# Kernel tuning notes

Hardware: AMD Instinct MI355X
Metric: run time of the kernel (lower is better)

Reference implementation:

```python
import jax, jax.numpy as jnp
import numpy as np


def _rank_transform_ascending(flat):
    # torch: _, idx = sort(flat, descending=False); flat[idx] = linspace(0,1,n)+1/n
    n = flat.shape[0]
    order = jnp.argsort(flat)  # ascending
    prob = jnp.linspace(0.0, 1.0, n, dtype=flat.dtype) + jnp.asarray(1.0 / n, flat.dtype)
    return jnp.zeros_like(flat).at[order].set(prob)


def corr_attention(query, key, value):
    # score[b,h,i,j] = cosine-like similarity q_i . k_j / (|q_i| |k_j|)
    score = jnp.einsum('bhid,bhjd->bhij', query, key)
    q_len = jnp.sqrt(jnp.sum(query * query, axis=-1, keepdims=True)) + 1e-5  # [b,h,s,1]
    k_len = jnp.sqrt(jnp.sum(key * key, axis=-1, keepdims=True)) + 1e-5      # [b,h,s,1]
    score = score / (q_len * jnp.swapaxes(k_len, -1, -2))
    signal = jnp.sign(score)
    size = score.shape
    flat = jnp.abs(score).reshape(-1)
    ranked = _rank_transform_ascending(flat)
    score = -jnp.log(ranked).reshape(size) * signal
    score = score / jnp.sum(jnp.abs(score), axis=-1, keepdims=True)
    return jnp.einsum('bhij,bhjd->bhid', score, value)


def setup_inputs() -> dict:
    key0 = jax.random.key(0)
    kq, kk, kv = jax.random.split(key0, 3)
    B, H, S, D = 4, 8, 1024, 64
    query = jax.random.normal(kq, (B, H, S, D), dtype=jnp.float32)
    key = jax.random.normal(kk, (B, H, S, D), dtype=jnp.float32)
    value = jax.random.normal(kv, (B, H, S, D), dtype=jnp.float32)
    return {"query": query, "key": key, "value": value}


def reference(query, key, value):
    # Attention.forward with mode='season'
    return corr_attention(query, key, value)
```

## Files before the change

kernel.cpp:

```cpp
#include <hip/hip_runtime.h>
#include <math.h>
#include <stdint.h>

#define S_LEN 1024
#define D_DIM 64
#define BH    32
#define KSHIFT 13
#define NBINS 130048u
#define HOT_LO 115712u
#define NHOT   14336u
#define HIST_LO 117760u
#define NHOT_H  12288u
#define NCHUNK 254
#define HBLK   256
#define INV_NM1 (1.0f/33554431.0f)
#define INV_N   (2.9802322387695312e-08f)
#define FIX_TH  1e-4f

typedef _Float16 half8 __attribute__((ext_vector_type(8)));
typedef short    short8 __attribute__((ext_vector_type(8)));
typedef float    floatx4 __attribute__((ext_vector_type(4)));

__global__ __launch_bounds__(256) void norms_kernel(
    const float* __restrict__ Q, const float* __restrict__ K,
    double* __restrict__ qinvD, double* __restrict__ kinvD,
    float* __restrict__ qinvF, float* __restrict__ kinvF) {
  int row  = blockIdx.x * 4 + (threadIdx.x >> 6);
  int lane = threadIdx.x & 63;
  const float* src; double* dstD; float* dstF; int r = row;
  if (row < BH * S_LEN) { src = Q; dstD = qinvD; dstF = qinvF; }
  else                  { src = K; dstD = kinvD; dstF = kinvF; r = row - BH * S_LEN; }
  double v = (double)src[(size_t)r * D_DIM + lane];
  double s = v * v;
  #pragma unroll
  for (int off = 32; off; off >>= 1) s += __shfl_down(s, off);
  if (lane == 0) {
    double inv = 1.0 / (sqrt(s) + 1e-5);
    dstD[r] = inv;
    dstF[r] = (float)inv;
  }
}

__device__ __forceinline__ void bf16_split(float x, short& hi, short& lo) {
  unsigned u = __float_as_uint(x);
  unsigned h = (u + 0x7FFFu + ((u >> 16) & 1u)) >> 16;
  float hf = __uint_as_float(h << 16);
  float lf = x - hf;
  hi = (short)h;
  lo = (short)(__float_as_uint(lf) >> 16);
}

__global__ __launch_bounds__(256) void qk_mfma_kernel(
    const float* __restrict__ Q, const float* __restrict__ K,
    const float* __restrict__ qinvF, const float* __restrict__ kinvF,
    float* __restrict__ score) {
  __shared__ short Qhi[64][72], Qlo[64][72];
  __shared__ short Khi[64][72], Klo[64][72];
  int bh = blockIdx.z;
  int i0 = blockIdx.y * 64;
  int j0 = blockIdx.x * 64;
  int tid = threadIdx.x;
  const float* Qb = Q + ((size_t)bh * S_LEN + i0) * D_DIM;
  const float* Kb = K + ((size_t)bh * S_LEN + j0) * D_DIM;
  #pragma unroll
  for (int l = 0; l < 4; ++l) {
    int idx4 = l * 256 + tid;
    int row  = idx4 >> 4;
    int c4   = idx4 & 15;
    float qi = qinvF[(size_t)bh * S_LEN + i0 + row];
    float4 v = ((const float4*)Qb)[idx4];
    float qv[4] = {v.x * qi, v.y * qi, v.z * qi, v.w * qi};
    short qh[4], ql[4];
    #pragma unroll
    for (int c = 0; c < 4; ++c) bf16_split(qv[c], qh[c], ql[c]);
    *(short4*)&Qhi[row][c4 * 4] = make_short4(qh[0], qh[1], qh[2], qh[3]);
    *(short4*)&Qlo[row][c4 * 4] = make_short4(ql[0], ql[1], ql[2], ql[3]);
    float kj = kinvF[(size_t)bh * S_LEN + j0 + row];
    float4 w = ((const float4*)Kb)[idx4];
    float kv[4] = {w.x * kj, w.y * kj, w.z * kj, w.w * kj};
    short kh[4], kl[4];
    #pragma unroll
    for (int c = 0; c < 4; ++c) bf16_split(kv[c], kh[c], kl[c]);
    *(short4*)&Khi[row][c4 * 4] = make_short4(kh[0], kh[1], kh[2], kh[3]);
    *(short4*)&Klo[row][c4 * 4] = make_short4(kl[0], kl[1], kl[2], kl[3]);
  }
  __syncthreads();
  int wave = tid >> 6;
  int lane = tid & 63;
  int m    = lane & 15;
  int quad = lane >> 4;
  floatx4 acc[4];
  #pragma unroll
  for (int n = 0; n < 4; ++n) acc[n] = (floatx4){0.f, 0.f, 0.f, 0.f};
  #pragma unroll
  for (int ks = 0; ks < 2; ++ks) {
    int kb = ks * 32 + quad * 8;
    short8 a_hi = *(const short8*)&Qhi[wave * 16 + m][kb];
    short8 a_lo = *(const short8*)&Qlo[wave * 16 + m][kb];
    #pragma unroll
    for (int nt = 0; nt < 4; ++nt) {
      short8 b_hi = *(const short8*)&Khi[nt * 16 + m][kb];
      short8 b_lo = *(const short8*)&Klo[nt * 16 + m][kb];
      acc[nt] = __builtin_amdgcn_mfma_f32_16x16x32_bf16(a_hi, b_hi, acc[nt], 0, 0, 0);
      acc[nt] = __builtin_amdgcn_mfma_f32_16x16x32_bf16(a_hi, b_lo, acc[nt], 0, 0, 0);
      acc[nt] = __builtin_amdgcn_mfma_f32_16x16x32_bf16(a_lo, b_hi, acc[nt], 0, 0, 0);
    }
  }
  #pragma unroll
  for (int r = 0; r < 4; ++r) {
    float* op = score + ((size_t)bh * S_LEN + i0 + wave * 16 + quad * 4 + r) * S_LEN + j0 + m;
    #pragma unroll
    for (int nt = 0; nt < 4; ++nt)
      op[nt * 16] = acc[nt][r];
  }
}

__global__ __launch_bounds__(1024) void hist_kernel(
    float* __restrict__ score, const float* __restrict__ Q, const float* __restrict__ K,
    const double* __restrict__ qinvD, const double* __restrict__ kinvD,
    unsigned* __restrict__ hist, unsigned char* __restrict__ partial) {
  __shared__ unsigned lh[NHOT_H];
  int tid = threadIdx.x;
  int lane = tid & 63;
  for (unsigned i = tid; i < NHOT_H; i += 1024) lh[i] = 0u;
  __syncthreads();
  const float4* p = (const float4*)score + (size_t)blockIdx.x * 32768;
  #pragma unroll 2
  for (int it = 0; it < 32; ++it) {
    float4 v = p[it * 1024 + tid];
    float vv[4] = {v.x, v.y, v.z, v.w};
    bool anyf = (fabsf(vv[0]) < FIX_TH) | (fabsf(vv[1]) < FIX_TH) |
                (fabsf(vv[2]) < FIX_TH) | (fabsf(vv[3]) < FIX_TH);
    unsigned long long am = __ballot(anyf);
    while (am) {
      int src = (int)(__ffsll((long long)am) - 1);
      am &= am - 1;
      unsigned base4 = (unsigned)(blockIdx.x * 32768u + (unsigned)(it * 1024 + tid));
      unsigned b4 = __shfl(base4, src);
      #pragma unroll
      for (int c = 0; c < 4; ++c) {
        float sc = __shfl(vv[c], src);
        if (fabsf(sc) < FIX_TH) {
          unsigned flat = b4 * 4u + (unsigned)c;
          unsigned bh = flat >> 20, i = (flat >> 10) & 1023u, j = flat & 1023u;
          double qd = (double)Q[((size_t)bh * S_LEN + i) * D_DIM + lane];
          double kd = (double)K[((size_t)bh * S_LEN + j) * D_DIM + lane];
          double pd = qd * kd;
          #pragma unroll
          for (int off = 32; off; off >>= 1) pd += __shfl_down(pd, off);
          float corr = 0.f;
          if (lane == 0)
            corr = (float)(pd * qinvD[(size_t)bh * S_LEN + i] * kinvD[(size_t)bh * S_LEN + j]);
          corr = __shfl(corr, 0);
          if (lane == src) {
            vv[c] = corr;
            score[(size_t)flat] = corr;
          }
        }
      }
    }
    #pragma unroll
    for (int c = 0; c < 4; ++c) {
      unsigned b = __float_as_uint(fabsf(vv[c])) >> KSHIFT;
      if (b >= NBINS) b = NBINS - 1u;
      if (b >= HIST_LO) atomicAdd(&lh[b - HIST_LO], 1u);
      else              atomicAdd(&hist[b], 1u);
    }
  }
  __syncthreads();
  unsigned char* dst = partial + (size_t)blockIdx.x * NHOT_H;
  for (unsigned i = tid; i < NHOT_H; i += 1024) dst[i] = (unsigned char)lh[i];
}

__global__ __launch_bounds__(256) void hreduce_kernel(
    const unsigned char* __restrict__ partial, unsigned* __restrict__ hist) {
  unsigned bin = blockIdx.x * 256 + threadIdx.x;
  unsigned s = 0;
  #pragma unroll 8
  for (int b = 0; b < HBLK; ++b) s += (unsigned)partial[(size_t)b * NHOT_H + bin];
  hist[HIST_LO + bin] = s;
}

__global__ __launch_bounds__(256) void vt_kernel(
    const float* __restrict__ V, _Float16* __restrict__ Vt) {
  __shared__ _Float16 T[64][72];
  int bh = blockIdx.y, j0 = blockIdx.x * 64, tid = threadIdx.x;
  const float* Vb = V + ((size_t)bh * S_LEN + j0) * D_DIM;
  #pragma unroll
  for (int l = 0; l < 4; ++l) {
    int idx = l * 256 + tid;
    int jr = idx >> 4, d4 = idx & 15;
    float4 v = ((const float4*)Vb)[idx];
    T[d4*4+0][jr] = (_Float16)v.x;
    T[d4*4+1][jr] = (_Float16)v.y;
    T[d4*4+2][jr] = (_Float16)v.z;
    T[d4*4+3][jr] = (_Float16)v.w;
  }
  __syncthreads();
  _Float16* Ob = Vt + (size_t)bh * D_DIM * S_LEN + j0;
  #pragma unroll
  for (int l = 0; l < 2; ++l) {
    int idx = l * 256 + tid;
    int d = idx >> 3, jc = idx & 7;
    uint4 val = *(const uint4*)&T[d][jc*8];
    *(uint4*)(Ob + (size_t)d * S_LEN + jc*8) = val;
  }
}

__global__ __launch_bounds__(256) void scan1_kernel(const unsigned* __restrict__ hist,
                                                    unsigned* __restrict__ csum) {
  __shared__ unsigned sd[256];
  int c = blockIdx.x, t = threadIdx.x;
  const unsigned* p = hist + (size_t)c * 512;
  sd[t] = p[t] + p[t + 256];
  __syncthreads();
  for (int off = 128; off; off >>= 1) {
    if (t < off) sd[t] += sd[t + off];
    __syncthreads();
  }
  if (t == 0) csum[c] = sd[0];
}

__global__ __launch_bounds__(256) void scan2_kernel(unsigned* __restrict__ csum) {
  __shared__ unsigned d[256];
  int t = threadIdx.x;
  unsigned v = (t < NCHUNK) ? csum[t] : 0u;
  d[t] = v; __syncthreads();
  for (int off = 1; off < 256; off <<= 1) {
    unsigned x = (t >= off) ? d[t - off] : 0u;
    __syncthreads();
    d[t] += x;
    __syncthreads();
  }
  if (t < NCHUNK) csum[t] = d[t] - v;
}

__global__ __launch_bounds__(256) void scan3_kernel(const unsigned* __restrict__ hist,
                                                    const unsigned* __restrict__ csum,
                                                    _Float16* __restrict__ tTab16) {
  __shared__ unsigned ts[256];
  int c = blockIdx.x, t = threadIdx.x;
  const unsigned* p = hist + (size_t)c * 512 + t * 2;
  unsigned l0 = p[0], l1 = p[1];
  unsigned s = l0 + l1;
  ts[t] = s; __syncthreads();
  for (int off = 1; off < 256; off <<= 1) {
    unsigned x = (t >= off) ? ts[t - off] : 0u;
    __syncthreads();
    ts[t] += x;
    __syncthreads();
  }
  unsigned base = csum[c] + ts[t] - s;
  int idx = c * 512 + t * 2;
  float r0 = (float)base + 0.5f * ((float)l0 - 1.0f);
  tTab16[idx]     = (_Float16)(-__logf(fmaf(r0, INV_NM1, INV_N)));
  float r1 = (float)(base + l0) + 0.5f * ((float)l1 - 1.0f);
  tTab16[idx + 1] = (_Float16)(-__logf(fmaf(r1, INV_NM1, INV_N)));
}

__global__ __launch_bounds__(256, 2) void pv_mfma_kernel(
    const float* __restrict__ score, const _Float16* __restrict__ Vt,
    const unsigned short* __restrict__ tTab16, float* __restrict__ out) {
  __shared__ unsigned short ldsT[NHOT];
  int tid = threadIdx.x;
  {
    const unsigned* gsrc = (const unsigned*)(tTab16 + HOT_LO);
    unsigned* ldst = (unsigned*)ldsT;
    #pragma unroll
    for (int i = 0; i < 28; ++i)
      ldst[i * 256 + tid] = gsrc[i * 256 + tid];
  }
  __syncthreads();

  int bh   = blockIdx.y;
  int wave = tid >> 6;
  int lane = tid & 63;
  int m    = lane & 15;
  int quad = lane >> 4;
  int i0   = blockIdx.x * 64 + wave * 16;
  const float*    Sb = score + ((size_t)bh * S_LEN + i0 + m) * S_LEN;
  const _Float16* Vb = Vt + (size_t)bh * D_DIM * S_LEN;
  floatx4 acc[4];
  #pragma unroll
  for (int n = 0; n < 4; ++n) acc[n] = (floatx4){0.f, 0.f, 0.f, 0.f};
  float rsum = 0.f;

  auto gather8 = [&](const float4& a, const float4& b, unsigned short* t8) {
    float sv[8] = {a.x, a.y, a.z, a.w, b.x, b.y, b.z, b.w};
    #pragma unroll
    for (int e = 0; e < 8; ++e) {
      unsigned u = __float_as_uint(sv[e]);
      unsigned av = u & 0x7fffffffu;
      unsigned bb = av >> KSHIFT;
      if (bb > NBINS - 1u) bb = NBINS - 1u;
      unsigned short tb;
      if (bb >= HOT_LO) tb = ldsT[bb - HOT_LO];
      else              tb = tTab16[bb];
      if (av == 0u) tb = 0;
      t8[e] = (unsigned short)(tb ^ ((u >> 16) & 0x8000u));
    }
  };

  float4 sc0[2], sc1[2];
  unsigned short tbs[2][8];
  half8 bfs[2][4];

  sc0[0] = *(const float4*)(Sb + quad * 8);
  sc1[0] = *(const float4*)(Sb + quad * 8 + 4);
  sc0[1] = *(const float4*)(Sb + 32 + quad * 8);
  sc1[1] = *(const float4*)(Sb + 32 + quad * 8 + 4);
  #pragma unroll
  for (int n = 0; n < 4; ++n)
    bfs[0][n] = *(const half8*)(Vb + (size_t)(n * 16 + m) * S_LEN + quad * 8);
  gather8(sc0[0], sc1[0], tbs[0]);

  #pragma unroll 2
  for (int ks = 0; ks < 32; ++ks) {
    const int cur = ks & 1, nxt = cur ^ 1;
    const int kN = (ks + 1) * 32 + quad * 8;
    const int kP = (ks + 2) * 32 + quad * 8;
    #pragma unroll
    for (int n = 0; n < 4; ++n)
      bfs[nxt][n] = *(const half8*)(Vb + (size_t)(n * 16 + m) * S_LEN + kN);
    gather8(sc0[nxt], sc1[nxt], tbs[nxt]);
    sc0[cur] = *(const float4*)(Sb + kP);
    sc1[cur] = *(const float4*)(Sb + kP + 4);
    union { unsigned short u[8]; half8 h; } af;
    #pragma unroll
    for (int e = 0; e < 8; ++e) {
      unsigned short tv = tbs[cur][e];
      af.u[e] = tv;
      _Float16 th = __builtin_bit_cast(_Float16, (unsigned short)(tv & 0x7fffu));
      rsum += (float)th;
    }
    #pragma unroll
    for (int n = 0; n < 4; ++n)
      acc[n] = __builtin_amdgcn_mfma_f32_16x16x32_f16(af.h, bfs[cur][n], acc[n], 0, 0, 0);
  }

  rsum += __shfl_xor(rsum, 16);
  rsum += __shfl_xor(rsum, 32);
  float inv = 1.0f / rsum;
  #pragma unroll
  for (int r = 0; r < 4; ++r) {
    int row = quad * 4 + r;
    float invr = __shfl(inv, row);
    float* op = out + ((size_t)bh * S_LEN + i0 + row) * D_DIM + m;
    #pragma unroll
    for (int n = 0; n < 4; ++n)
      op[n * 16] = acc[n][r] * invr;
  }
}

extern "C" void kernel_launch(void* const* d_in, const int* in_sizes, int n_in,
                              void* d_out, int out_size, void* d_ws, size_t ws_size,
                              hipStream_t stream) {
  const float* Q = (const float*)d_in[0];
  const float* K = (const float*)d_in[1];
  const float* V = (const float*)d_in[2];
  float* out = (float*)d_out;
  char* ws = (char*)d_ws;
  float*         score   = (float*)(ws);
  unsigned*      hist    = (unsigned*)(ws + 134217728);
  unsigned char* partial = (unsigned char*)(ws + 134737920);
  double*        qinvD   = (double*)(ws + 137883648);
  double*        kinvD   = (double*)(ws + 138145792);
  float*         qinvF   = (float*)(ws + 138407936);
  float*         kinvF   = (float*)(ws + 138539008);
  _Float16*      Vt      = (_Float16*)(ws + 134737920);
  unsigned*      csum    = (unsigned*)(ws + 139194368);
  _Float16*      tTab16  = (_Float16*)(ws + 139195392);

  hipMemsetAsync(hist, 0, NBINS * sizeof(unsigned), stream);
  norms_kernel<<<(2 * BH * S_LEN) / 4, 256, 0, stream>>>(Q, K, qinvD, kinvD, qinvF, kinvF);
  qk_mfma_kernel<<<dim3(16, 16, BH), 256, 0, stream>>>(Q, K, qinvF, kinvF, score);
  hist_kernel<<<HBLK, 1024, 0, stream>>>(score, Q, K, qinvD, kinvD, hist, partial);
  hreduce_kernel<<<NHOT_H / 256, 256, 0, stream>>>(partial, hist);
  vt_kernel<<<dim3(16, BH), 256, 0, stream>>>(V, Vt);
  scan1_kernel<<<NCHUNK, 256, 0, stream>>>(hist, csum);
  scan2_kernel<<<1, 256, 0, stream>>>(csum);
  scan3_kernel<<<NCHUNK, 256, 0, stream>>>(hist, csum, tTab16);
  pv_mfma_kernel<<<dim3(16, BH), 256, 0, stream>>>(
      score, Vt, (const unsigned short*)tTab16, out);
}
```

Baseline: 219.7 us.

## Fuse QK score computation with histogram pass in one kernel

Merges the QK^T MFMA kernel and the histogram kernel. Each 512-thread block now owns a 64-row Q tile and loops over all K tiles. The histogram and near-zero fixups run on register-resident scores, so the separate pass that re-read the full 128MB score matrix is gone. The shared-memory histogram packs two 16-bit counters per word to fit occupancy. The cost is 512 smaller grid blocks, a serialized K loop with syncs per tile, a larger partial array to reduce, and per-block counts that could overflow the byte-sized partial entries.

After: 229.3 us. +4.4%, slower.

```diff
diff --git a/kernel.cpp b/kernel.cpp
--- a/kernel.cpp
+++ b/kernel.cpp
@@ -12,7 +12,7 @@
 #define HIST_LO 117760u
 #define NHOT_H  12288u
 #define NCHUNK 254
-#define HBLK   256
+#define QHB    512
 #define INV_NM1 (1.0f/33554431.0f)
 #define INV_N   (2.9802322387695312e-08f)
 #define FIX_TH  1e-4f
@@ -50,21 +50,23 @@
   lo = (short)(__float_as_uint(lf) >> 16);
 }
 
-__global__ __launch_bounds__(256) void qk_mfma_kernel(
+__global__ __launch_bounds__(512, 4) void qkhist_kernel(
     const float* __restrict__ Q, const float* __restrict__ K,
     const float* __restrict__ qinvF, const float* __restrict__ kinvF,
-    float* __restrict__ score) {
+    const double* __restrict__ qinvD, const double* __restrict__ kinvD,
+    float* __restrict__ score, unsigned* __restrict__ hist,
+    unsigned char* __restrict__ partial) {
   __shared__ short Qhi[64][72], Qlo[64][72];
   __shared__ short Khi[64][72], Klo[64][72];
-  int bh = blockIdx.z;
-  int i0 = blockIdx.y * 64;
-  int j0 = blockIdx.x * 64;
+  __shared__ unsigned lh[NHOT_H / 2];
   int tid = threadIdx.x;
+  int bh  = blockIdx.x >> 4;
+  int i0  = (blockIdx.x & 15) * 64;
+  for (unsigned i = tid; i < NHOT_H / 2; i += 512) lh[i] = 0u;
   const float* Qb = Q + ((size_t)bh * S_LEN + i0) * D_DIM;
-  const float* Kb = K + ((size_t)bh * S_LEN + j0) * D_DIM;
-  #pragma unroll
-  for (int l = 0; l < 4; ++l) {
-    int idx4 = l * 256 + tid;
+  #pragma unroll
+  for (int l = 0; l < 2; ++l) {
+    int idx4 = l * 512 + tid;
     int row  = idx4 >> 4;
     int c4   = idx4 & 15;
     float qi = qinvF[(size_t)bh * S_LEN + i0 + row];
@@ -75,101 +77,109 @@
     for (int c = 0; c < 4; ++c) bf16_split(qv[c], qh[c], ql[c]);
     *(short4*)&Qhi[row][c4 * 4] = make_short4(qh[0], qh[1], qh[2], qh[3]);
     *(short4*)&Qlo[row][c4 * 4] = make_short4(ql[0], ql[1], ql[2], ql[3]);
-    float kj = kinvF[(size_t)bh * S_LEN + j0 + row];
-    float4 w = ((const float4*)Kb)[idx4];
-    float kv[4] = {w.x * kj, w.y * kj, w.z * kj, w.w * kj};
-    short kh[4], kl[4];
-    #pragma unroll
-    for (int c = 0; c < 4; ++c) bf16_split(kv[c], kh[c], kl[c]);
-    *(short4*)&Khi[row][c4 * 4] = make_short4(kh[0], kh[1], kh[2], kh[3]);
-    *(short4*)&Klo[row][c4 * 4] = make_short4(kl[0], kl[1], kl[2], kl[3]);
-  }
-  __syncthreads();
+  }
   int wave = tid >> 6;
   int lane = tid & 63;
   int m    = lane & 15;
   int quad = lane >> 4;
-  floatx4 acc[4];
-  #pragma unroll
-  for (int n = 0; n < 4; ++n) acc[n] = (floatx4){0.f, 0.f, 0.f, 0.f};
-  #pragma unroll
-  for (int ks = 0; ks < 2; ++ks) {
-    int kb = ks * 32 + quad * 8;
-    short8 a_hi = *(const short8*)&Qhi[wave * 16 + m][kb];
-    short8 a_lo = *(const short8*)&Qlo[wave * 16 + m][kb];
-    #pragma unroll
-    for (int nt = 0; nt < 4; ++nt) {
-      short8 b_hi = *(const short8*)&Khi[nt * 16 + m][kb];
-      short8 b_lo = *(const short8*)&Klo[nt * 16 + m][kb];
-      acc[nt] = __builtin_amdgcn_mfma_f32_16x16x32_bf16(a_hi, b_hi, acc[nt], 0, 0, 0);
-      acc[nt] = __builtin_amdgcn_mfma_f32_16x16x32_bf16(a_hi, b_lo, acc[nt], 0, 0, 0);
-      acc[nt] = __builtin_amdgcn_mfma_f32_16x16x32_bf16(a_lo, b_hi, acc[nt], 0, 0, 0);
-    }
-  }
-  #pragma unroll
-  for (int r = 0; r < 4; ++r) {
-    float* op = score + ((size_t)bh * S_LEN + i0 + wave * 16 + quad * 4 + r) * S_LEN + j0 + m;
-    #pragma unroll
-    for (int nt = 0; nt < 4; ++nt)
-      op[nt * 16] = acc[nt][r];
-  }
-}
-
-__global__ __launch_bounds__(1024) void hist_kernel(
-    float* __restrict__ score, const float* __restrict__ Q, const float* __restrict__ K,
-    const double* __restrict__ qinvD, const double* __restrict__ kinvD,
-    unsigned* __restrict__ hist, unsigned char* __restrict__ partial) {
-  __shared__ unsigned lh[NHOT_H];
-  int tid = threadIdx.x;
-  int lane = tid & 63;
-  for (unsigned i = tid; i < NHOT_H; i += 1024) lh[i] = 0u;
-  __syncthreads();
-  const float4* p = (const float4*)score + (size_t)blockIdx.x * 32768;
-  #pragma unroll 2
-  for (int it = 0; it < 32; ++it) {
-    float4 v = p[it * 1024 + tid];
-    float vv[4] = {v.x, v.y, v.z, v.w};
-    bool anyf = (fabsf(vv[0]) < FIX_TH) | (fabsf(vv[1]) < FIX_TH) |
-                (fabsf(vv[2]) < FIX_TH) | (fabsf(vv[3]) < FIX_TH);
+  int g    = wave >> 1;
+  int h    = wave & 1;
+
+  for (int jt = 0; jt < 16; ++jt) {
+    int j0 = jt * 64;
+    __syncthreads();
+    const float* Kb = K + ((size_t)bh * S_LEN + j0) * D_DIM;
+    #pragma unroll
+    for (int l = 0; l < 2; ++l) {
+      int idx4 = l * 512 + tid;
+      int row  = idx4 >> 4;
+      int c4   = idx4 & 15;
+      float kj = kinvF[(size_t)bh * S_LEN + j0 + row];
+      float4 w = ((const float4*)Kb)[idx4];
+      float kv[4] = {w.x * kj, w.y * kj, w.z * kj, w.w * kj};
+      short kh[4], kl[4];
+      #pragma unroll
+      for (int c = 0; c < 4; ++c) bf16_split(kv[c], kh[c], kl[c]);
+      *(short4*)&Khi[row][c4 * 4] = make_short4(kh[0], kh[1], kh[2], kh[3]);
+      *(short4*)&Klo[row][c4 * 4] = make_short4(kl[0], kl[1], kl[2], kl[3]);
+    }
+    __syncthreads();
+    floatx4 acc[2];
+    acc[0] = (floatx4){0.f, 0.f, 0.f, 0.f};
+    acc[1] = (floatx4){0.f, 0.f, 0.f, 0.f};
+    #pragma unroll
+    for (int ks = 0; ks < 2; ++ks) {
+      int kb = ks * 32 + quad * 8;
+      short8 a_hi = *(const short8*)&Qhi[g * 16 + m][kb];
+      short8 a_lo = *(const short8*)&Qlo[g * 16 + m][kb];
+      #pragma unroll
+      for (int t = 0; t < 2; ++t) {
+        int nt = h * 2 + t;
+        short8 b_hi = *(const short8*)&Khi[nt * 16 + m][kb];
+        short8 b_lo = *(const short8*)&Klo[nt * 16 + m][kb];
+        acc[t] = __builtin_amdgcn_mfma_f32_16x16x32_bf16(a_hi, b_hi, acc[t], 0, 0, 0);
+        acc[t] = __builtin_amdgcn_mfma_f32_16x16x32_bf16(a_hi, b_lo, acc[t], 0, 0, 0);
+        acc[t] = __builtin_amdgcn_mfma_f32_16x16x32_bf16(a_lo, b_hi, acc[t], 0, 0, 0);
+      }
+    }
+    float sv[8];
+    #pragma unroll
+    for (int t = 0; t < 2; ++t)
+      #pragma unroll
+      for (int r = 0; r < 4; ++r) sv[t * 4 + r] = acc[t][r];
+
+    bool anyf = false;
+    #pragma unroll
+    for (int e = 0; e < 8; ++e) anyf |= (fabsf(sv[e]) < FIX_TH);
     unsigned long long am = __ballot(anyf);
     while (am) {
       int src = (int)(__ffsll((long long)am) - 1);
       am &= am - 1;
-      unsigned base4 = (unsigned)(blockIdx.x * 32768u + (unsigned)(it * 1024 + tid));
-      unsigned b4 = __shfl(base4, src);
       #pragma unroll
-      for (int c = 0; c < 4; ++c) {
-        float sc = __shfl(vv[c], src);
+      for (int e = 0; e < 8; ++e) {
+        float sc = __shfl(sv[e], src);
         if (fabsf(sc) < FIX_TH) {
-          unsigned flat = b4 * 4u + (unsigned)c;
-          unsigned bh = flat >> 20, i = (flat >> 10) & 1023u, j = flat & 1023u;
-          double qd = (double)Q[((size_t)bh * S_LEN + i) * D_DIM + lane];
-          double kd = (double)K[((size_t)bh * S_LEN + j) * D_DIM + lane];
+          int t = e >> 2, r = e & 3;
+          int row = i0 + g * 16 + ((src >> 4)) * 4 + r;
+          int col = j0 + (h * 2 + t) * 16 + (src & 15);
+          double qd = (double)Q[((size_t)bh * S_LEN + row) * D_DIM + lane];
+          double kd = (double)K[((size_t)bh * S_LEN + col) * D_DIM + lane];
           double pd = qd * kd;
           #pragma unroll
           for (int off = 32; off; off >>= 1) pd += __shfl_down(pd, off);
           float corr = 0.f;
           if (lane == 0)
-            corr = (float)(pd * qinvD[(size_t)bh * S_LEN + i] * kinvD[(size_t)bh * S_LEN + j]);
+            corr = (float)(pd * qinvD[(size_t)bh * S_LEN + row] * kinvD[(size_t)bh * S_LEN + col]);
           corr = __shfl(corr, 0);
-          if (lane == src) {
-            vv[c] = corr;
-            score[(size_t)flat] = corr;
-          }
+          if (lane == src) sv[e] = corr;
         }
       }
     }
     #pragma unroll
-    for (int c = 0; c < 4; ++c) {
-      unsigned b = __float_as_uint(fabsf(vv[c])) >> KSHIFT;
+    for (int r = 0; r < 4; ++r) {
+      float* op = score + ((size_t)bh * S_LEN + i0 + g * 16 + quad * 4 + r) * S_LEN + j0 + m;
+      op[(h * 2 + 0) * 16] = sv[r];
+      op[(h * 2 + 1) * 16] = sv[4 + r];
+    }
+    #pragma unroll
+    for (int e = 0; e < 8; ++e) {
+      unsigned b = __float_as_uint(fabsf(sv[e])) >> KSHIFT;
       if (b >= NBINS) b = NBINS - 1u;
-      if (b >= HIST_LO) atomicAdd(&lh[b - HIST_LO], 1u);
-      else              atomicAdd(&hist[b], 1u);
+      if (b >= HIST_LO) {
+        unsigned bb = b - HIST_LO;
+        atomicAdd(&lh[bb >> 1], (bb & 1u) ? 65536u : 1u);
+      } else {
+        atomicAdd(&hist[b], 1u);
+      }
     }
   }
   __syncthreads();
   unsigned char* dst = partial + (size_t)blockIdx.x * NHOT_H;
-  for (unsigned i = tid; i < NHOT_H; i += 1024) dst[i] = (unsigned char)lh[i];
+  for (unsigned i = tid; i < NHOT_H / 2; i += 512) {
+    unsigned w = lh[i];
+    dst[2 * i]     = (unsigned char)(w & 0xffffu);
+    dst[2 * i + 1] = (unsigned char)(w >> 16);
+  }
 }
 
 __global__ __launch_bounds__(256) void hreduce_kernel(
@@ -177,7 +187,7 @@
   unsigned bin = blockIdx.x * 256 + threadIdx.x;
   unsigned s = 0;
   #pragma unroll 8
-  for (int b = 0; b < HBLK; ++b) s += (unsigned)partial[(size_t)b * NHOT_H + bin];
+  for (int b = 0; b < QHB; ++b) s += (unsigned)partial[(size_t)b * NHOT_H + bin];
   hist[HIST_LO + bin] = s;
 }
 
@@ -363,18 +373,18 @@
   float*         score   = (float*)(ws);
   unsigned*      hist    = (unsigned*)(ws + 134217728);
   unsigned char* partial = (unsigned char*)(ws + 134737920);
-  double*        qinvD   = (double*)(ws + 137883648);
-  double*        kinvD   = (double*)(ws + 138145792);
-  float*         qinvF   = (float*)(ws + 138407936);
-  float*         kinvF   = (float*)(ws + 138539008);
-  _Float16*      Vt      = (_Float16*)(ws + 134737920);
   unsigned*      csum    = (unsigned*)(ws + 139194368);
   _Float16*      tTab16  = (_Float16*)(ws + 139195392);
+  _Float16*      Vt      = (_Float16*)(ws + 134737920);
+  double*        qinvD   = (double*)(ws + 141029376);
+  double*        kinvD   = (double*)(ws + 141291520);
+  float*         qinvF   = (float*)(ws + 141553664);
+  float*         kinvF   = (float*)(ws + 141684736);
 
   hipMemsetAsync(hist, 0, NBINS * sizeof(unsigned), stream);
   norms_kernel<<<(2 * BH * S_LEN) / 4, 256, 0, stream>>>(Q, K, qinvD, kinvD, qinvF, kinvF);
-  qk_mfma_kernel<<<dim3(16, 16, BH), 256, 0, stream>>>(Q, K, qinvF, kinvF, score);
-  hist_kernel<<<HBLK, 1024, 0, stream>>>(score, Q, K, qinvD, kinvD, hist, partial);
+  qkhist_kernel<<<QHB, 512, 0, stream>>>(Q, K, qinvF, kinvF, qinvD, kinvD,
+                                         score, hist, partial);
   hreduce_kernel<<<NHOT_H / 256, 256, 0, stream>>>(partial, hist);
   vt_kernel<<<dim3(16, BH), 256, 0, stream>>>(V, Vt);
   scan1_kernel<<<NCHUNK, 256, 0, stream>>>(hist, csum);
```
